# Kernel tuning notes

Hardware: AMD Instinct MI355X
Metric: run time of the kernel (lower is better)

Reference implementation:

```python
import jax, jax.numpy as jnp
import numpy as np

B, D = 1024, 512


def setup_inputs() -> dict:
    key = jax.random.key(0)
    k1, k2, k3 = jax.random.split(key, 3)
    x = jax.random.normal(k1, (B, D), dtype=jnp.float32)
    x_dot = jax.random.normal(k2, (B, D), dtype=jnp.float32)
    # linear score network weight: s(x) = x @ W^T  (scaled for sane magnitudes)
    W = jax.random.normal(k3, (D, D), dtype=jnp.float32) / np.sqrt(D).astype(np.float32)
    return {"x": x, "x_dot": x_dot, "W": W}


def reference(x, x_dot, W):
    # s(x): [b, d]
    s = x @ W.T
    d = x.shape[1]
    # g(x) = I + s s^T : [b, d, d]  (faithful to the original bmm formulation)
    G = jnp.eye(d, dtype=x.dtype)[None, :, :] + s[:, :, None] * s[:, None, :]
    # kinetic energy: x_dot^T G x_dot : [b]
    return jnp.einsum('bi,bij,bj->b', x_dot, G, x_dot)
```

## Files before the change

kernel.cpp:

```cpp
#include <hip/hip_runtime.h>

#define BB 1024
#define DD 512
#define BTILE 32
#define JTILE 128
#define ICH 64
#define NIC (DD / ICH)
#define NTP ((DD / JTILE) * NIC)
#define NNP (NIC * 4)

__global__ __launch_bounds__(256, 4) void stm_main_kernel(
    const float* __restrict__ x, const float* __restrict__ xdot,
    const float* __restrict__ W, float* __restrict__ ws_t) {
  __shared__ float xd_t[ICH][BTILE];
  __shared__ float w_s[ICH][JTILE];

  const int tid = threadIdx.x;
  const int b0 = blockIdx.x * BTILE;
  const int j0 = blockIdx.y * JTILE;
  const int i0 = blockIdx.z * ICH;
  const int tb = tid >> 5;
  const int tj = tid & 31;

  float nrm = 0.f;
  {
    const int row = tid & 31;
    const int f4 = tid >> 5;
    const float4* src = (const float4*)(xdot + (size_t)(b0 + row) * DD + i0);
#pragma unroll
    for (int p = 0; p < 2; ++p) {
      const int c4 = f4 + p * 8;
      float4 v = src[c4];
      nrm += v.x * v.x + v.y * v.y + v.z * v.z + v.w * v.w;
      const int c = c4 * 4;
      xd_t[c + 0][row] = v.x; xd_t[c + 1][row] = v.y;
      xd_t[c + 2][row] = v.z; xd_t[c + 3][row] = v.w;
    }
  }
  {
#pragma unroll
    for (int v = 0; v < 8; ++v) {
      const int f4 = tid + v * 256;
      const int ii = f4 >> 5, jj4 = f4 & 31;
      *((float4*)&w_s[ii][jj4 * 4]) =
          ((const float4*)(W + (size_t)(i0 + ii) * DD + j0))[jj4];
    }
  }

  if (blockIdx.y == 0) {
    nrm += __shfl_xor(nrm, 32);
    const int wv = tid >> 6, ln = tid & 63;
    if (ln < 32)
      ws_t[(size_t)(NTP + blockIdx.z * 4 + wv) * BB + b0 + ln] = nrm;
  }

  float4 xv[4];
#pragma unroll
  for (int r = 0; r < 4; ++r)
    xv[r] = ((const float4*)(x + (size_t)(b0 + tb * 4 + r) * DD + j0))[tj];

  __syncthreads();

  float acc[4][4] = {};
#pragma unroll
  for (int i = 0; i < ICH; ++i) {
    const float4 xd = *(const float4*)&xd_t[i][tb * 4];
    const float4 w  = *(const float4*)&w_s[i][tj * 4];
    acc[0][0] += xd.x * w.x; acc[0][1] += xd.x * w.y;
    acc[0][2] += xd.x * w.z; acc[0][3] += xd.x * w.w;
    acc[1][0] += xd.y * w.x; acc[1][1] += xd.y * w.y;
    acc[1][2] += xd.y * w.z; acc[1][3] += xd.y * w.w;
    acc[2][0] += xd.z * w.x; acc[2][1] += xd.z * w.y;
    acc[2][2] += xd.z * w.z; acc[2][3] += xd.z * w.w;
    acc[3][0] += xd.w * w.x; acc[3][1] += xd.w * w.y;
    acc[3][2] += xd.w * w.z; acc[3][3] += xd.w * w.w;
  }

  float tp[4];
#pragma unroll
  for (int r = 0; r < 4; ++r)
    tp[r] = acc[r][0] * xv[r].x + acc[r][1] * xv[r].y +
            acc[r][2] * xv[r].z + acc[r][3] * xv[r].w;
#pragma unroll
  for (int off = 16; off >= 1; off >>= 1) {
#pragma unroll
    for (int r = 0; r < 4; ++r) tp[r] += __shfl_xor(tp[r], off);
  }
  if (tj == 0) {
    const int p = blockIdx.y * NIC + blockIdx.z;
    *(float4*)(ws_t + (size_t)p * BB + b0 + tb * 4) =
        make_float4(tp[0], tp[1], tp[2], tp[3]);
  }
}

__global__ __launch_bounds__(256) void stm_final_kernel(
    const float* __restrict__ ws_t, float* __restrict__ out) {
  const int b = blockIdx.x * 256 + threadIdx.x;
  float t = 0.f, n = 0.f;
#pragma unroll
  for (int p = 0; p < NTP; ++p) t += ws_t[(size_t)p * BB + b];
#pragma unroll
  for (int p = 0; p < NNP; ++p) n += ws_t[(size_t)(NTP + p) * BB + b];
  out[b] = n + t * t;
}

extern "C" void kernel_launch(void* const* d_in, const int* in_sizes, int n_in,
                              void* d_out, int out_size, void* d_ws, size_t ws_size,
                              hipStream_t stream) {
  const float* x    = (const float*)d_in[0];
  const float* xdot = (const float*)d_in[1];
  const float* W    = (const float*)d_in[2];
  float* ws = (float*)d_ws;
  float* out = (float*)d_out;

  dim3 g1(BB / BTILE, DD / JTILE, NIC);
  stm_main_kernel<<<g1, 256, 0, stream>>>(x, xdot, W, ws);
  stm_final_kernel<<<BB / 256, 256, 0, stream>>>(ws, out);
}
```

Before: 68.51 us.

## Fuse final reduction into main kernel via last-block atomic counter and double batch tile

Removes the separate reduction kernel. Each batch tile now has a per-tile atomic counter, and the last of its 32 contributing blocks sums the partial results and writes the output. The batch tile also grows from 32 to 64 rows, so each thread holds 8x4 accumulators. That halves the grid size and the number of norm partials. The counter sits in workspace that is never reset and relies on modulo-32 wraparound, so it depends on the workspace starting at zero. The larger tile also lowers the number of blocks and the occupancy target.

```diff
diff --git a/kernel.cpp b/kernel.cpp
--- a/kernel.cpp
+++ b/kernel.cpp
@@ -2,18 +2,22 @@
 
 #define BB 1024
 #define DD 512
-#define BTILE 32
+#define BTILE 64
 #define JTILE 128
 #define ICH 64
 #define NIC (DD / ICH)
 #define NTP ((DD / JTILE) * NIC)
-#define NNP (NIC * 4)
+#define NNP NIC
+#define NROWS (NTP + NNP)
+#define XDLD (BTILE + 4)
 
-__global__ __launch_bounds__(256, 4) void stm_main_kernel(
+__global__ __launch_bounds__(256, 2) void stm_fused_kernel(
     const float* __restrict__ x, const float* __restrict__ xdot,
-    const float* __restrict__ W, float* __restrict__ ws_t) {
-  __shared__ float xd_t[ICH][BTILE];
+    const float* __restrict__ W, float* __restrict__ ws,
+    float* __restrict__ out) {
+  __shared__ float xd_t[ICH][XDLD];
   __shared__ float w_s[ICH][JTILE];
+  __shared__ int last_flag;
 
   const int tid = threadIdx.x;
   const int b0 = blockIdx.x * BTILE;
@@ -22,14 +26,16 @@
   const int tb = tid >> 5;
   const int tj = tid & 31;
 
+  unsigned int* cnt = (unsigned int*)(ws + (size_t)NROWS * BB);
+
   float nrm = 0.f;
   {
-    const int row = tid & 31;
-    const int f4 = tid >> 5;
+    const int row = tid >> 2;
+    const int q = tid & 3;
     const float4* src = (const float4*)(xdot + (size_t)(b0 + row) * DD + i0);
 #pragma unroll
-    for (int p = 0; p < 2; ++p) {
-      const int c4 = f4 + p * 8;
+    for (int p = 0; p < 4; ++p) {
+      const int c4 = q + p * 4;
       float4 v = src[c4];
       nrm += v.x * v.x + v.y * v.y + v.z * v.z + v.w * v.w;
       const int c = c4 * 4;
@@ -48,60 +54,77 @@
   }
 
   if (blockIdx.y == 0) {
-    nrm += __shfl_xor(nrm, 32);
-    const int wv = tid >> 6, ln = tid & 63;
-    if (ln < 32)
-      ws_t[(size_t)(NTP + blockIdx.z * 4 + wv) * BB + b0 + ln] = nrm;
+    nrm += __shfl_xor(nrm, 1);
+    nrm += __shfl_xor(nrm, 2);
+    if ((tid & 3) == 0)
+      ws[(size_t)(NTP + blockIdx.z) * BB + b0 + (tid >> 2)] = nrm;
   }
 
-  float4 xv[4];
+  float4 xv[8];
 #pragma unroll
-  for (int r = 0; r < 4; ++r)
-    xv[r] = ((const float4*)(x + (size_t)(b0 + tb * 4 + r) * DD + j0))[tj];
+  for (int r = 0; r < 8; ++r)
+    xv[r] = ((const float4*)(x + (size_t)(b0 + tb * 8 + r) * DD + j0))[tj];
 
   __syncthreads();
 
-  float acc[4][4] = {};
+  float acc[8][4] = {};
 #pragma unroll
   for (int i = 0; i < ICH; ++i) {
-    const float4 xd = *(const float4*)&xd_t[i][tb * 4];
+    const float4 xa = *(const float4*)&xd_t[i][tb * 8];
+    const float4 xb = *(const float4*)&xd_t[i][tb * 8 + 4];
     const float4 w  = *(const float4*)&w_s[i][tj * 4];
-    acc[0][0] += xd.x * w.x; acc[0][1] += xd.x * w.y;
-    acc[0][2] += xd.x * w.z; acc[0][3] += xd.x * w.w;
-    acc[1][0] += xd.y * w.x; acc[1][1] += xd.y * w.y;
-    acc[1][2] += xd.y * w.z; acc[1][3] += xd.y * w.w;
-    acc[2][0] += xd.z * w.x; acc[2][1] += xd.z * w.y;
-    acc[2][2] += xd.z * w.z; acc[2][3] += xd.z * w.w;
-    acc[3][0] += xd.w * w.x; acc[3][1] += xd.w * w.y;
-    acc[3][2] += xd.w * w.z; acc[3][3] += xd.w * w.w;
+    const float xr[8] = {xa.x, xa.y, xa.z, xa.w, xb.x, xb.y, xb.z, xb.w};
+#pragma unroll
+    for (int r = 0; r < 8; ++r) {
+      acc[r][0] += xr[r] * w.x; acc[r][1] += xr[r] * w.y;
+      acc[r][2] += xr[r] * w.z; acc[r][3] += xr[r] * w.w;
+    }
   }
 
-  float tp[4];
+  float tp[8];
 #pragma unroll
-  for (int r = 0; r < 4; ++r)
+  for (int r = 0; r < 8; ++r)
     tp[r] = acc[r][0] * xv[r].x + acc[r][1] * xv[r].y +
             acc[r][2] * xv[r].z + acc[r][3] * xv[r].w;
 #pragma unroll
   for (int off = 16; off >= 1; off >>= 1) {
 #pragma unroll
-    for (int r = 0; r < 4; ++r) tp[r] += __shfl_xor(tp[r], off);
+    for (int r = 0; r < 8; ++r) tp[r] += __shfl_xor(tp[r], off);
   }
   if (tj == 0) {
     const int p = blockIdx.y * NIC + blockIdx.z;
-    *(float4*)(ws_t + (size_t)p * BB + b0 + tb * 4) =
-        make_float4(tp[0], tp[1], tp[2], tp[3]);
+    float* dst = ws + (size_t)p * BB + b0 + tb * 8;
+    *(float4*)(dst + 0) = make_float4(tp[0], tp[1], tp[2], tp[3]);
+    *(float4*)(dst + 4) = make_float4(tp[4], tp[5], tp[6], tp[7]);
   }
-}
 
-__global__ __launch_bounds__(256) void stm_final_kernel(
-    const float* __restrict__ ws_t, float* __restrict__ out) {
-  const int b = blockIdx.x * 256 + threadIdx.x;
-  float t = 0.f, n = 0.f;
+  __threadfence();
+  __syncthreads();
+  if (tid == 0) {
+    unsigned int old = atomicAdd(cnt + blockIdx.x, 1u);
+    last_flag = ((old & 31u) == 31u);
+  }
+  __syncthreads();
+  if (last_flag) {
+    __threadfence();
+    const int bl = tid & 63, g = tid >> 6;
+    float ts = 0.f, ns = 0.f;
 #pragma unroll
-  for (int p = 0; p < NTP; ++p) t += ws_t[(size_t)p * BB + b];
+    for (int k = 0; k < 8; ++k)
+      ts += ws[(size_t)(g * 8 + k) * BB + b0 + bl];
 #pragma unroll
-  for (int p = 0; p < NNP; ++p) n += ws_t[(size_t)(NTP + p) * BB + b];
-  out[b] = n + t * t;
+    for (int k = 0; k < 2; ++k)
+      ns += ws[(size_t)(NTP + g * 2 + k) * BB + b0 + bl];
+    float* red = (float*)xd_t;
+    red[g * 64 + bl] = ts;
+    red[256 + g * 64 + bl] = ns;
+    __syncthreads();
+    if (tid < 64) {
+      const float t = red[tid] + red[64 + tid] + red[128 + tid] + red[192 + tid];
+      const float n = red[256 + tid] + red[320 + tid] + red[384 + tid] + red[448 + tid];
+      out[b0 + tid] = n + t * t;
+    }
+  }
 }
 
 extern "C" void kernel_launch(void* const* d_in, const int* in_sizes, int n_in,
@@ -114,6 +137,5 @@
   float* out = (float*)d_out;
 
   dim3 g1(BB / BTILE, DD / JTILE, NIC);
-  stm_main_kernel<<<g1, 256, 0, stream>>>(x, xdot, W, ws);
-  stm_final_kernel<<<BB / 256, 256, 0, stream>>>(ws, out);
+  stm_fused_kernel<<<g1, 256, 0, stream>>>(x, xdot, W, ws, out);
 }
```

Result: slower. 97.37 us (+42.1%).
